# Performance work log

Hardware: AMD Instinct MI355X
Metric: run time of the kernel (lower is better)

## Reference

```python
import jax, jax.numpy as jnp
import numpy as np

B, N, D, H = 8, 2048, 512, 512


def setup_inputs() -> dict:
    key = jax.random.key(0)
    kx, kwq, kbq, kwk, kbk = jax.random.split(key, 5)
    s = 1.0 / np.sqrt(D)
    return {
        "x": jax.random.normal(kx, (B, N, D), dtype=jnp.float32),
        "Wq": jax.random.uniform(kwq, (D, H), jnp.float32, -s, s),
        "bq": jax.random.uniform(kbq, (H,), jnp.float32, -s, s),
        "Wk": jax.random.uniform(kwk, (D, H), jnp.float32, -s, s),
        "bk": jax.random.uniform(kbk, (H,), jnp.float32, -s, s),
    }


def reference(x, Wq, bq, Wk, bk):
    # x: [B, N, D]
    q = jnp.einsum("bnd,dh->bnh", x, Wq) + bq          # [B, N, H]
    k = jnp.einsum("bnd,dh->bnh", x, Wk) + bk          # [B, N, H]
    energy = jnp.einsum("bih,bjh->bij", q, k)           # [B, N, N] (no scaling)
    # NOTE: softmax over dim=1 (the QUERY axis), not the usual key axis.
    attn = jax.nn.softmax(energy, axis=1)               # [B, N, N]
    out = jnp.einsum("bij,bjd->bid", attn, x)           # V = x
    return out
```

## Files before the change

### kernel.cpp

```cpp
#include <hip/hip_runtime.h>
#include <hip/hip_bf16.h>
#include <cstdio>

typedef float f32x4 __attribute__((ext_vector_type(4)));
typedef __bf16 bf16x8 __attribute__((ext_vector_type(8)));

static constexpr int Bn = 8, Nn = 2048, Dn = 512, Hn = 512;

__device__ __forceinline__ unsigned short f2bf(float x) {
    union { float f; unsigned int u; } v; v.f = x;
    unsigned int r = (v.u + 0x7FFFu + ((v.u >> 16) & 1u)) >> 16;
    return (unsigned short)r;
}
__device__ __forceinline__ float bf2f(unsigned short h) {
    union { unsigned int u; float f; } v; v.u = ((unsigned int)h) << 16;
    return v.f;
}

__device__ __forceinline__ void gload_lds16(const unsigned short* g, unsigned short* l) {
    __builtin_amdgcn_global_load_lds(
        (const __attribute__((address_space(1))) void*)g,
        (__attribute__((address_space(3))) void*)l,
        16, 0, 0);
}

__device__ __forceinline__ int xcd_swizzle(int lin, int nwg) {
    return (lin & 7) * (nwg >> 3) + (lin >> 3);
}

__global__ void cast_x_kernel(const float* __restrict__ x, unsigned short* __restrict__ xb, int n) {
    int i = (blockIdx.x * blockDim.x + threadIdx.x) * 8;
    if (i >= n) return;
    float4 a = *(const float4*)(x + i);
    float4 b = *(const float4*)(x + i + 4);
    unsigned short tmp[8] = {f2bf(a.x), f2bf(a.y), f2bf(a.z), f2bf(a.w),
                             f2bf(b.x), f2bf(b.y), f2bf(b.z), f2bf(b.w)};
    *(uint4*)(xb + i) = *(const uint4*)tmp;
}

__global__ __launch_bounds__(256) void transpose_cast_kernel(
    const float* __restrict__ in, unsigned short* __restrict__ out,
    const float* __restrict__ sdiv, int R, int C)
{
    __shared__ float tile[64][65];
    const int z = blockIdx.z;
    const float* inb = in + (size_t)z * R * C;
    unsigned short* outb = out + (size_t)z * R * C;
    const int r0 = blockIdx.y * 64, c0 = blockIdx.x * 64;
    const int tx = threadIdx.x & 63, ty = threadIdx.x >> 6;
#pragma unroll
    for (int p = 0; p < 64; p += 4) {
        const int r = p + ty;
        float v = inb[(size_t)(r0 + r) * C + c0 + tx];
        if (sdiv) v /= sdiv[(size_t)z * R + r0 + r];
        tile[r][tx] = v;
    }
    __syncthreads();
#pragma unroll
    for (int p = 0; p < 64; p += 4) {
        const int oc = p + ty;
        outb[(size_t)(c0 + oc) * R + r0 + tx] = f2bf(tile[tx][oc]);
    }
}

__global__ void combine_s_kernel(const float* __restrict__ s_part, float* __restrict__ s,
                                 int nblk, int total) {
    int i = blockIdx.x * blockDim.x + threadIdx.x;
    if (i >= total) return;
    int z = i >> 11, j = i & (Nn - 1);
    float acc = 0.f;
    for (int p = 0; p < nblk; ++p) acc += s_part[((size_t)z * nblk + p) * Nn + j];
    s[i] = acc;
}

template<int MODE>
__global__ __launch_bounds__(512, 2) void gemm8p(
    const unsigned short* __restrict__ A, long long sA, int lda,
    const unsigned short* __restrict__ Bt, long long sB, int ldb,
    void* __restrict__ Cp, long long sC,
    const float* __restrict__ bias, const float* __restrict__ bias2, int bsplit,
    float* __restrict__ s_part,
    int M, int N, int K, int gx, int gy)
{
    __shared__ unsigned short As[4][8192];
    __shared__ unsigned short Bs[4][8192];

    const int lin = xcd_swizzle(blockIdx.x, gridDim.x);
    const int bz = lin / (gx * gy);
    const int rem = lin - bz * gx * gy;
    const int by = rem / gx;
    const int bx = rem - by * gx;

    const unsigned short* Ab = A + (size_t)bz * sA;
    const unsigned short* Bb = Bt + (size_t)bz * sB;
    const int i0 = by * 256, j0 = bx * 256;

    const int t = threadIdx.x;
    const int lane = t & 63;
    const int w = t >> 6;
    const int wm = w >> 2, wn = w & 3;
    const int l15 = lane & 15, g = lane >> 4;

    const int rd_off = (l15 * 4 + (g ^ ((l15 >> 1) & 3))) * 16;
    const int grow = lane >> 2;
    const int gk = ((lane & 3) ^ ((lane >> 3) & 3)) * 8;

    f32x4 acc[8][4];
    const f32x4 zero4 = {0.f, 0.f, 0.f, 0.f};
#pragma unroll
    for (int mi = 0; mi < 8; ++mi)
#pragma unroll
        for (int nf = 0; nf < 4; ++nf) acc[mi][nf] = zero4;

    const int NT = K >> 6;

#define STAGE(baseP, ldP, r0P, ldsP, Tn, kh)                                             \
    {                                                                                    \
        const int _slot = ((Tn) & 1) * 2 + (kh);                                         \
        const unsigned short* _src = (baseP) + (size_t)((r0P) + w * 16 + grow) * (ldP)   \
                                     + (Tn) * 64 + (kh) * 32 + gk;                       \
        gload_lds16(_src, &ldsP[_slot][w * 512]);                                        \
        gload_lds16(_src + (size_t)128 * (ldP), &ldsP[_slot][(w + 8) * 512]);            \
    }

    STAGE(Ab, lda, i0, As, 0, 0);
    STAGE(Bb, ldb, j0, Bs, 0, 0);
    STAGE(Ab, lda, i0, As, 0, 1);
    STAGE(Bb, ldb, j0, Bs, 0, 1);

    for (int T = 0; T < NT; ++T) {
        const int sbase = (T & 1) * 2;
        const bool last = (T == NT - 1);

        asm volatile("s_waitcnt vmcnt(4)" ::: "memory");
        asm volatile("s_barrier" ::: "memory");
        {
            const char* Bbase = (const char*)&Bs[sbase][0] + wn * 4096 + rd_off;
            const char* Abase = (const char*)&As[sbase][0] + wm * 8192 + rd_off;
            bf16x8 bfv[4], af[4];
#pragma unroll
            for (int nf = 0; nf < 4; ++nf) bfv[nf] = *(const bf16x8*)(Bbase + nf * 1024);
#pragma unroll
            for (int mf = 0; mf < 4; ++mf) af[mf] = *(const bf16x8*)(Abase + mf * 1024);
            if (!last) STAGE(Ab, lda, i0, As, T + 1, 0);
            __builtin_amdgcn_s_setprio(1);
#pragma unroll
            for (int mf = 0; mf < 4; ++mf)
#pragma unroll
                for (int nf = 0; nf < 4; ++nf)
                    acc[mf][nf] = __builtin_amdgcn_mfma_f32_16x16x32_bf16(af[mf], bfv[nf], acc[mf][nf], 0, 0, 0);
            __builtin_amdgcn_s_setprio(0);
            bf16x8 ag[4];
#pragma unroll
            for (int mf = 0; mf < 4; ++mf) ag[mf] = *(const bf16x8*)(Abase + 4096 + mf * 1024);
            if (!last) STAGE(Bb, ldb, j0, Bs, T + 1, 0);
            __builtin_amdgcn_s_setprio(1);
#pragma unroll
            for (int mf = 0; mf < 4; ++mf)
#pragma unroll
                for (int nf = 0; nf < 4; ++nf)
                    acc[4 + mf][nf] = __builtin_amdgcn_mfma_f32_16x16x32_bf16(ag[mf], bfv[nf], acc[4 + mf][nf], 0, 0, 0);
            __builtin_amdgcn_s_setprio(0);
        }

        if (last) asm volatile("s_waitcnt vmcnt(0)" ::: "memory");
        else      asm volatile("s_waitcnt vmcnt(4)" ::: "memory");
        asm volatile("s_barrier" ::: "memory");
        {
            const char* Bbase = (const char*)&Bs[sbase + 1][0] + wn * 4096 + rd_off;
            const char* Abase = (const char*)&As[sbase + 1][0] + wm * 8192 + rd_off;
            bf16x8 bfv[4], af[4];
#pragma unroll
            for (int nf = 0; nf < 4; ++nf) bfv[nf] = *(const bf16x8*)(Bbase + nf * 1024);
#pragma unroll
            for (int mf = 0; mf < 4; ++mf) af[mf] = *(const bf16x8*)(Abase + mf * 1024);
            if (!last) STAGE(Ab, lda, i0, As, T + 1, 1);
            __builtin_amdgcn_s_setprio(1);
#pragma unroll
            for (int mf = 0; mf < 4; ++mf)
#pragma unroll
                for (int nf = 0; nf < 4; ++nf)
                    acc[mf][nf] = __builtin_amdgcn_mfma_f32_16x16x32_bf16(af[mf], bfv[nf], acc[mf][nf], 0, 0, 0);
            __builtin_amdgcn_s_setprio(0);
            bf16x8 ag[4];
#pragma unroll
            for (int mf = 0; mf < 4; ++mf) ag[mf] = *(const bf16x8*)(Abase + 4096 + mf * 1024);
            if (!last) STAGE(Bb, ldb, j0, Bs, T + 1, 1);
            __builtin_amdgcn_s_setprio(1);
#pragma unroll
            for (int mf = 0; mf < 4; ++mf)
#pragma unroll
                for (int nf = 0; nf < 4; ++nf)
                    acc[4 + mf][nf] = __builtin_amdgcn_mfma_f32_16x16x32_bf16(ag[mf], bfv[nf], acc[4 + mf][nf], 0, 0, 0);
            __builtin_amdgcn_s_setprio(0);
        }
    }
#undef STAGE

    if (MODE == 0) {
        unsigned short* C = (unsigned short*)Cp;
        float bv[4];
#pragma unroll
        for (int nf = 0; nf < 4; ++nf) {
            const int col = j0 + wn * 64 + nf * 16 + l15;
            bv[nf] = (col < bsplit) ? bias[col] : bias2[col - bsplit];
        }
        const int col0 = j0 + wn * 64 + l15;
#pragma unroll
        for (int mi = 0; mi < 8; ++mi) {
            const int rb = i0 + wm * 128 + (mi >> 2) * 64 + (mi & 3) * 16 + g * 4;
#pragma unroll
            for (int r = 0; r < 4; ++r) {
                unsigned short* Crow = C + (size_t)(rb + r) * N + col0;
#pragma unroll
                for (int nf = 0; nf < 4; ++nf)
                    Crow[nf * 16] = f2bf(acc[mi][nf][r] + bv[nf]);
            }
        }
    } else {
        unsigned short* C = (unsigned short*)Cp + (size_t)bz * sC;
        float cs[4] = {0.f, 0.f, 0.f, 0.f};
        const int col0 = j0 + wn * 64 + l15;
#pragma unroll
        for (int mi = 0; mi < 8; ++mi) {
            const int rb = i0 + wm * 128 + (mi >> 2) * 64 + (mi & 3) * 16 + g * 4;
#pragma unroll
            for (int r = 0; r < 4; ++r) {
                unsigned short* Crow = C + (size_t)(rb + r) * N + col0;
#pragma unroll
                for (int nf = 0; nf < 4; ++nf) {
                    const float e = __expf(acc[mi][nf][r]);
                    const unsigned short h = f2bf(e);
                    Crow[nf * 16] = h;
                    cs[nf] += bf2f(h);
                }
            }
        }
#pragma unroll
        for (int nf = 0; nf < 4; ++nf) {
            cs[nf] += __shfl_xor(cs[nf], 16);
            cs[nf] += __shfl_xor(cs[nf], 32);
        }
        __syncthreads();
        float* red = (float*)&As[0][0];
        if (g == 0) {
#pragma unroll
            for (int nf = 0; nf < 4; ++nf)
                red[wm * 256 + wn * 64 + nf * 16 + l15] = cs[nf];
        }
        __syncthreads();
        if (t < 256)
            s_part[((size_t)bz * gy + by) * Nn + j0 + t] = red[t] + red[256 + t];
    }
}

__global__ __launch_bounds__(256, 2) void gemm_pv(
    const unsigned short* __restrict__ A, long long sA, int lda,
    const unsigned short* __restrict__ Bt, long long sB, int ldb,
    float* __restrict__ Cp, long long sC,
    int M, int N, int K, int gx, int gy)
{
    __shared__ unsigned short As[2][128 * 64];
    __shared__ unsigned short Bs[2][128 * 64];

    const int lin = xcd_swizzle(blockIdx.x, gridDim.x);
    const int bz = lin / (gx * gy);
    const int rem = lin - bz * gx * gy;
    const int by = rem / gx;
    const int bx = rem - by * gx;

    const unsigned short* Ab = A + (size_t)bz * sA;
    const unsigned short* Bb = Bt + (size_t)bz * sB;
    const int i0 = by * 128, j0 = bx * 128;

    const int t = threadIdx.x;
    const int lane = t & 63;
    const int wave = t >> 6;
    const int wr = wave >> 1, wc = wave & 1;
    const int l15 = lane & 15, g = lane >> 4;

    f32x4 acc[4][4];
    const f32x4 zero4 = {0.f, 0.f, 0.f, 0.f};
#pragma unroll
    for (int mi = 0; mi < 4; ++mi)
#pragma unroll
        for (int ni = 0; ni < 4; ++ni) acc[mi][ni] = zero4;

    const int rbase = wave * 32;
    const int lrow = lane >> 3;
    const int gch = (lane & 7) ^ lrow;

#define STAGEPV(s, ktv)                                                        \
    {                                                                          \
        _Pragma("unroll")                                                      \
        for (int i = 0; i < 4; ++i) {                                          \
            const int r = rbase + i * 8 + lrow;                                \
            gload_lds16(Ab + (size_t)(i0 + r) * lda + (ktv) + gch * 8,         \
                        &As[s][(rbase + i * 8) * 64]);                         \
            gload_lds16(Bb + (size_t)(j0 + r) * ldb + (ktv) + gch * 8,         \
                        &Bs[s][(rbase + i * 8) * 64]);                         \
        }                                                                      \
    }

    STAGEPV(0, 0);
    asm volatile("s_waitcnt vmcnt(0)" ::: "memory");
    asm volatile("s_barrier" ::: "memory");

    const int NT = K >> 6;
    for (int T = 0; T < NT; ++T) {
        const int cur = T & 1;
        if (T + 1 < NT) STAGEPV(cur ^ 1, (T + 1) * 64);
#pragma unroll
        for (int kk = 0; kk < 64; kk += 32) {
            const int sl0 = (kk >> 3) + g;
            bf16x8 af[4], bfr[4];
#pragma unroll
            for (int mi = 0; mi < 4; ++mi) {
                const int row = wr * 64 + mi * 16 + l15;
                af[mi] = *(const bf16x8*)(&As[cur][0] + row * 64 + ((sl0 ^ (row & 7)) * 8));
            }
#pragma unroll
            for (int ni = 0; ni < 4; ++ni) {
                const int row = wc * 64 + ni * 16 + l15;
                bfr[ni] = *(const bf16x8*)(&Bs[cur][0] + row * 64 + ((sl0 ^ (row & 7)) * 8));
            }
            __builtin_amdgcn_s_setprio(1);
#pragma unroll
            for (int mi = 0; mi < 4; ++mi)
#pragma unroll
                for (int ni = 0; ni < 4; ++ni)
                    acc[mi][ni] = __builtin_amdgcn_mfma_f32_16x16x32_bf16(af[mi], bfr[ni], acc[mi][ni], 0, 0, 0);
            __builtin_amdgcn_s_setprio(0);
        }
        asm volatile("s_waitcnt vmcnt(0)" ::: "memory");
        asm volatile("s_barrier" ::: "memory");
    }
#undef STAGEPV

    float* C = Cp + (size_t)bz * sC;
#pragma unroll
    for (int ni = 0; ni < 4; ++ni) {
        const int col = j0 + wc * 64 + ni * 16 + l15;
#pragma unroll
        for (int mi = 0; mi < 4; ++mi) {
            const int rb = i0 + wr * 64 + mi * 16 + g * 4;
#pragma unroll
            for (int r = 0; r < 4; ++r)
                C[(size_t)(rb + r) * N + col] = acc[mi][ni][r];
        }
    }
}

extern "C" void kernel_launch(void* const* d_in, const int* in_sizes, int n_in,
                              void* d_out, int out_size, void* d_ws, size_t ws_size,
                              hipStream_t stream) {
    const float* x  = (const float*)d_in[0];
    const float* Wq = (const float*)d_in[1];
    const float* bq = (const float*)d_in[2];
    const float* Wk = (const float*)d_in[3];
    const float* bk = (const float*)d_in[4];
    float* out = (float*)d_out;

    char* ws = (char*)d_ws;
    unsigned short* xb    = (unsigned short*)(ws);
    unsigned short* qk    = (unsigned short*)(ws + (16ull << 20));
    unsigned short* WqkT  = (unsigned short*)(ws + (48ull << 20));
    unsigned short* xsT   = (unsigned short*)(ws + (49ull << 20));
    float*          s_prt = (float*)(ws + (65ull << 20));
    float*          s     = (float*)(ws + (66ull << 20));
    unsigned short* expE  = (unsigned short*)(ws + (67ull << 20));
    if (ws_size < (131ull << 20)) {
        fprintf(stderr, "WS TOO SMALL: have %zu need %llu\n", ws_size, (131ull << 20));
    }

    cast_x_kernel<<<dim3((Bn * Nn * Dn) / (8 * 256)), 256, 0, stream>>>(x, xb, Bn * Nn * Dn);
    transpose_cast_kernel<<<dim3(Hn / 64, Dn / 64, 1), 256, 0, stream>>>(Wq, WqkT, nullptr, Dn, Hn);
    transpose_cast_kernel<<<dim3(Hn / 64, Dn / 64, 1), 256, 0, stream>>>(Wk, WqkT + (size_t)Hn * Dn, nullptr, Dn, Hn);
    {
        const int gx = (2 * Hn) / 256, gy = (Bn * Nn) / 256;
        gemm8p<0><<<dim3(gx * gy), 512, 0, stream>>>(
            xb, 0, Dn, WqkT, 0, Dn, qk, 0, bq, bk, Hn, nullptr,
            Bn * Nn, 2 * Hn, Dn, gx, gy);
    }
    {
        const int gx = Nn / 256, gy = Nn / 256;
        gemm8p<1><<<dim3(gx * gy * Bn), 512, 0, stream>>>(
            qk, (long long)Nn * 2 * Hn, 2 * Hn,
            qk + Hn, (long long)Nn * 2 * Hn, 2 * Hn,
            expE, (long long)Nn * Nn, nullptr, nullptr, 0, s_prt,
            Nn, Nn, Hn, gx, gy);
    }
    combine_s_kernel<<<dim3((Bn * Nn) / 256), 256, 0, stream>>>(s_prt, s, Nn / 256, Bn * Nn);
    transpose_cast_kernel<<<dim3(Dn / 64, Nn / 64, Bn), 256, 0, stream>>>(x, xsT, s, Nn, Dn);
    {
        const int gx = Dn / 128, gy = Nn / 128;
        gemm_pv<<<dim3(gx * gy * Bn), 256, 0, stream>>>(
            expE, (long long)Nn * Nn, Nn, xsT, (long long)Dn * Nn, Nn,
            out, (long long)Nn * Dn, Nn, Dn, Nn, gx, gy);
    }
}
```

Measured before the change: 144.2 us.

## Restructure 256x256 GEMM main loop into eight-phase pipeline with finer LDS staging

Replaces the two-phase-per-K-tile loop of the 256x256 bf16 GEMM with an 8-phase schedule over two K-tiles. Each phase interleaves half-tile global-to-LDS loads with a quarter of the MFMA work, separated by explicit barriers and sched_barrier. LDS is re-laid out into row halves with a new XOR swizzle, and launch bounds drop from 2 to 1 blocks per CU, giving the compiler more registers. The aim is better overlap of memory loads with MFMA and fewer LDS bank conflicts, at the cost of more barriers and lower occupancy.

```diff
diff --git a/kernel.cpp b/kernel.cpp
--- a/kernel.cpp
+++ b/kernel.cpp
@@ -74,7 +74,7 @@
 }
 
 template<int MODE>
-__global__ __launch_bounds__(512, 2) void gemm8p(
+__global__ __launch_bounds__(512, 1) void gemm8m(
     const unsigned short* __restrict__ A, long long sA, int lda,
     const unsigned short* __restrict__ Bt, long long sB, int ldb,
     void* __restrict__ Cp, long long sC,
@@ -82,8 +82,8 @@
     float* __restrict__ s_part,
     int M, int N, int K, int gx, int gy)
 {
-    __shared__ unsigned short As[4][8192];
-    __shared__ unsigned short Bs[4][8192];
+    __shared__ unsigned short As[2][2][8192];
+    __shared__ unsigned short Bs[2][2][8192];
 
     const int lin = xcd_swizzle(blockIdx.x, gridDim.x);
     const int bz = lin / (gx * gy);
@@ -101,9 +101,15 @@
     const int wm = w >> 2, wn = w & 3;
     const int l15 = lane & 15, g = lane >> 4;
 
-    const int rd_off = (l15 * 4 + (g ^ ((l15 >> 1) & 3))) * 16;
-    const int grow = lane >> 2;
-    const int gk = ((lane & 3) ^ ((lane >> 3) & 3)) * 8;
+    const int ro  = (l15 >> 3) * 1024 + (l15 & 7) * 128;
+    const int sw0 = (g ^ (l15 & 7)) * 16;
+    const int sw1 = sw0 ^ 64;
+    const char* Ahalf = (const char*)&As[0][wm][0];
+    const char* Bhalf = (const char*)&Bs[0][wn >> 1][0];
+    const int bofs = (wn & 1) * 8192;
+
+    const int lrow = lane >> 3;
+    const int gch = (lane & 7) ^ lrow;
 
     f32x4 acc[8][4];
     const f32x4 zero4 = {0.f, 0.f, 0.f, 0.f};
@@ -114,88 +120,75 @@
 
     const int NT = K >> 6;
 
-#define STAGE(baseP, ldP, r0P, ldsP, Tn, kh)                                             \
-    {                                                                                    \
-        const int _slot = ((Tn) & 1) * 2 + (kh);                                         \
-        const unsigned short* _src = (baseP) + (size_t)((r0P) + w * 16 + grow) * (ldP)   \
-                                     + (Tn) * 64 + (kh) * 32 + gk;                       \
-        gload_lds16(_src, &ldsP[_slot][w * 512]);                                        \
-        gload_lds16(_src + (size_t)128 * (ldP), &ldsP[_slot][(w + 8) * 512]);            \
-    }
-
-    STAGE(Ab, lda, i0, As, 0, 0);
-    STAGE(Bb, ldb, j0, Bs, 0, 0);
-    STAGE(Ab, lda, i0, As, 0, 1);
-    STAGE(Bb, ldb, j0, Bs, 0, 1);
-
-    for (int T = 0; T < NT; ++T) {
-        const int sbase = (T & 1) * 2;
-        const bool last = (T == NT - 1);
-
-        asm volatile("s_waitcnt vmcnt(4)" ::: "memory");
-        asm volatile("s_barrier" ::: "memory");
-        {
-            const char* Bbase = (const char*)&Bs[sbase][0] + wn * 4096 + rd_off;
-            const char* Abase = (const char*)&As[sbase][0] + wm * 8192 + rd_off;
-            bf16x8 bfv[4], af[4];
-#pragma unroll
-            for (int nf = 0; nf < 4; ++nf) bfv[nf] = *(const bf16x8*)(Bbase + nf * 1024);
-#pragma unroll
-            for (int mf = 0; mf < 4; ++mf) af[mf] = *(const bf16x8*)(Abase + mf * 1024);
-            if (!last) STAGE(Ab, lda, i0, As, T + 1, 0);
-            __builtin_amdgcn_s_setprio(1);
-#pragma unroll
-            for (int mf = 0; mf < 4; ++mf)
-#pragma unroll
-                for (int nf = 0; nf < 4; ++nf)
-                    acc[mf][nf] = __builtin_amdgcn_mfma_f32_16x16x32_bf16(af[mf], bfv[nf], acc[mf][nf], 0, 0, 0);
-            __builtin_amdgcn_s_setprio(0);
-            bf16x8 ag[4];
-#pragma unroll
-            for (int mf = 0; mf < 4; ++mf) ag[mf] = *(const bf16x8*)(Abase + 4096 + mf * 1024);
-            if (!last) STAGE(Bb, ldb, j0, Bs, T + 1, 0);
-            __builtin_amdgcn_s_setprio(1);
-#pragma unroll
-            for (int mf = 0; mf < 4; ++mf)
-#pragma unroll
-                for (int nf = 0; nf < 4; ++nf)
-                    acc[4 + mf][nf] = __builtin_amdgcn_mfma_f32_16x16x32_bf16(ag[mf], bfv[nf], acc[4 + mf][nf], 0, 0, 0);
-            __builtin_amdgcn_s_setprio(0);
-        }
-
-        if (last) asm volatile("s_waitcnt vmcnt(0)" ::: "memory");
-        else      asm volatile("s_waitcnt vmcnt(4)" ::: "memory");
-        asm volatile("s_barrier" ::: "memory");
-        {
-            const char* Bbase = (const char*)&Bs[sbase + 1][0] + wn * 4096 + rd_off;
-            const char* Abase = (const char*)&As[sbase + 1][0] + wm * 8192 + rd_off;
-            bf16x8 bfv[4], af[4];
-#pragma unroll
-            for (int nf = 0; nf < 4; ++nf) bfv[nf] = *(const bf16x8*)(Bbase + nf * 1024);
-#pragma unroll
-            for (int mf = 0; mf < 4; ++mf) af[mf] = *(const bf16x8*)(Abase + mf * 1024);
-            if (!last) STAGE(Ab, lda, i0, As, T + 1, 1);
-            __builtin_amdgcn_s_setprio(1);
-#pragma unroll
-            for (int mf = 0; mf < 4; ++mf)
-#pragma unroll
-                for (int nf = 0; nf < 4; ++nf)
-                    acc[mf][nf] = __builtin_amdgcn_mfma_f32_16x16x32_bf16(af[mf], bfv[nf], acc[mf][nf], 0, 0, 0);
-            __builtin_amdgcn_s_setprio(0);
-            bf16x8 ag[4];
-#pragma unroll
-            for (int mf = 0; mf < 4; ++mf) ag[mf] = *(const bf16x8*)(Abase + 4096 + mf * 1024);
-            if (!last) STAGE(Bb, ldb, j0, Bs, T + 1, 1);
-            __builtin_amdgcn_s_setprio(1);
-#pragma unroll
-            for (int mf = 0; mf < 4; ++mf)
-#pragma unroll
-                for (int nf = 0; nf < 4; ++nf)
-                    acc[4 + mf][nf] = __builtin_amdgcn_mfma_f32_16x16x32_bf16(ag[mf], bfv[nf], acc[4 + mf][nf], 0, 0, 0);
-            __builtin_amdgcn_s_setprio(0);
-        }
-    }
-#undef STAGE
+#define STAGE_A(d, h, Tn)                                                            \
+    {                                                                                \
+        const unsigned short* _s = Ab + (size_t)(i0 + (h) * 128 + w * 16 + lrow) * lda \
+                                   + (Tn) * 64 + gch * 8;                            \
+        gload_lds16(_s, &As[d][h][w * 1024]);                                        \
+        gload_lds16(_s + (size_t)8 * lda, &As[d][h][w * 1024 + 512]);                \
+    }
+#define STAGE_B(d, h, Tn)                                                            \
+    {                                                                                \
+        const unsigned short* _s = Bb + (size_t)(j0 + (h) * 128 + w * 16 + lrow) * ldb \
+                                   + (Tn) * 64 + gch * 8;                            \
+        gload_lds16(_s, &Bs[d][h][w * 1024]);                                        \
+        gload_lds16(_s + (size_t)8 * ldb, &Bs[d][h][w * 1024 + 512]);                \
+    }
+
+#define PHASE(d, kk, mh, STG, VMW)                                                   \
+    {                                                                                \
+        if ((mh) == 0) {                                                             \
+            _Pragma("unroll") for (int nf = 0; nf < 4; ++nf)                         \
+                bfv[nf] = *(const bf16x8*)(Bhalf + (d) * 32768 + bofs + nf * 2048    \
+                                           + ro + ((kk) ? sw1 : sw0));               \
+        }                                                                            \
+        bf16x8 af[4];                                                                \
+        _Pragma("unroll") for (int mf = 0; mf < 4; ++mf)                             \
+            af[mf] = *(const bf16x8*)(Ahalf + (d) * 32768 + (mh) * 8192 + mf * 2048  \
+                                      + ro + ((kk) ? sw1 : sw0));                    \
+        STG;                                                                         \
+        VMW;                                                                         \
+        __builtin_amdgcn_s_barrier();                                                \
+        asm volatile("s_waitcnt lgkmcnt(0)" ::: "memory");                           \
+        __builtin_amdgcn_sched_barrier(0);                                           \
+        __builtin_amdgcn_s_setprio(1);                                               \
+        _Pragma("unroll") for (int mf = 0; mf < 4; ++mf)                             \
+            _Pragma("unroll") for (int nf = 0; nf < 4; ++nf)                         \
+                acc[(mh) * 4 + mf][nf] = __builtin_amdgcn_mfma_f32_16x16x32_bf16(    \
+                    af[mf], bfv[nf], acc[(mh) * 4 + mf][nf], 0, 0, 0);               \
+        __builtin_amdgcn_s_setprio(0);                                               \
+        __builtin_amdgcn_s_barrier();                                                \
+    }
+
+#define VMC2 { if (sN) asm volatile("s_waitcnt vmcnt(2)" ::: "memory"); \
+               else    asm volatile("s_waitcnt vmcnt(0)" ::: "memory"); }
+
+    STAGE_B(0, 0, 0);
+    STAGE_A(0, 0, 0);
+    STAGE_A(0, 1, 0);
+    STAGE_B(0, 1, 0);
+    STAGE_B(1, 0, 1);
+    asm volatile("s_waitcnt vmcnt(2)" ::: "memory");
+    __builtin_amdgcn_s_barrier();
+
+    bf16x8 bfv[4];
+    const int NI = NT >> 1;
+    for (int I = 0; I < NI; ++I) {
+        const int tA = 2 * I + 1, tB = 2 * I + 2, tC = 2 * I + 3;
+        const bool sN = tB < NT;
+        PHASE(0, 0, 0, STAGE_B(1, 1, tA), {});
+        PHASE(0, 0, 1, STAGE_A(1, 0, tA), {});
+        PHASE(0, 1, 0, STAGE_A(1, 1, tA), {});
+        PHASE(0, 1, 1, if (sN) STAGE_B(0, 0, tB), VMC2);
+        PHASE(1, 0, 0, if (sN) STAGE_A(0, 0, tB), {});
+        PHASE(1, 0, 1, if (sN) STAGE_A(0, 1, tB), {});
+        PHASE(1, 1, 0, if (sN) STAGE_B(0, 1, tB), {});
+        PHASE(1, 1, 1, if (sN) STAGE_B(1, 0, tC), VMC2);
+    }
+#undef PHASE
+#undef STAGE_A
+#undef STAGE_B
+#undef VMC2
 
     if (MODE == 0) {
         unsigned short* C = (unsigned short*)Cp;
@@ -242,7 +235,7 @@
             cs[nf] += __shfl_xor(cs[nf], 32);
         }
         __syncthreads();
-        float* red = (float*)&As[0][0];
+        float* red = (float*)&As[0][0][0];
         if (g == 0) {
 #pragma unroll
             for (int nf = 0; nf < 4; ++nf)
@@ -378,13 +371,13 @@
     transpose_cast_kernel<<<dim3(Hn / 64, Dn / 64, 1), 256, 0, stream>>>(Wk, WqkT + (size_t)Hn * Dn, nullptr, Dn, Hn);
     {
         const int gx = (2 * Hn) / 256, gy = (Bn * Nn) / 256;
-        gemm8p<0><<<dim3(gx * gy), 512, 0, stream>>>(
+        gemm8m<0><<<dim3(gx * gy), 512, 0, stream>>>(
             xb, 0, Dn, WqkT, 0, Dn, qk, 0, bq, bk, Hn, nullptr,
             Bn * Nn, 2 * Hn, Dn, gx, gy);
     }
     {
         const int gx = Nn / 256, gy = Nn / 256;
-        gemm8p<1><<<dim3(gx * gy * Bn), 512, 0, stream>>>(
+        gemm8m<1><<<dim3(gx * gy * Bn), 512, 0, stream>>>(
             qk, (long long)Nn * 2 * Hn, 2 * Hn,
             qk + Hn, (long long)Nn * 2 * Hn, 2 * Hn,
             expE, (long long)Nn * Nn, nullptr, nullptr, 0, s_prt,
```

Result: no change. 145.0 us (+0.6%).
